# Optimization experiments

Hardware: AMD Instinct MI355X
Metric: run time of the kernel (lower is better)

Reference implementation:

```python
import jax, jax.numpy as jnp
import numpy as np

PAIR = 128
HID = 64
EPS = 1e-5


def _ln(x, w, b):
    mu = jnp.mean(x, axis=-1, keepdims=True)
    var = jnp.mean((x - mu) ** 2, axis=-1, keepdims=True)
    return (x - mu) * jax.lax.rsqrt(var + EPS) * w + b


def setup_inputs() -> dict:
    key = jax.random.key(0)
    ks = jax.random.split(key, 8)
    B, N = 1, 448
    s_in = 1.0 / np.sqrt(PAIR)
    s_h = 1.0 / np.sqrt(HID)
    return {
        "z": jax.random.normal(ks[0], (B, N, N, PAIR), jnp.float32),
        "z_mask": jnp.ones((B, N, N), jnp.float32),
        "ln_w": jnp.ones((PAIR,), jnp.float32),
        "ln_b": jnp.zeros((PAIR,), jnp.float32),
        "lnh_w": jnp.ones((HID,), jnp.float32),
        "lnh_b": jnp.zeros((HID,), jnp.float32),
        "g1_w": jax.random.uniform(ks[1], (PAIR, HID), jnp.float32, -s_in, s_in),
        "g1_b": jnp.zeros((HID,), jnp.float32),
        "g2_w": jax.random.uniform(ks[2], (PAIR, HID), jnp.float32, -s_in, s_in),
        "g2_b": jnp.zeros((HID,), jnp.float32),
        "l1_w": jax.random.uniform(ks[3], (PAIR, HID), jnp.float32, -s_in, s_in),
        "l1_b": jnp.zeros((HID,), jnp.float32),
        "l2_w": jax.random.uniform(ks[4], (PAIR, HID), jnp.float32, -s_in, s_in),
        "l2_b": jnp.zeros((HID,), jnp.float32),
        "eg_w": jax.random.uniform(ks[5], (PAIR, PAIR), jnp.float32, -s_in, s_in),
        "eg_b": jnp.zeros((PAIR,), jnp.float32),
        "out_w": jax.random.uniform(ks[6], (HID, PAIR), jnp.float32, -s_h, s_h),
        "out_b": jnp.zeros((PAIR,), jnp.float32),
    }


def reference(z, z_mask, ln_w, ln_b, lnh_w, lnh_b, g1_w, g1_b, g2_w, g2_b,
              l1_w, l1_b, l2_w, l2_b, eg_w, eg_b, out_w, out_b):
    m = z_mask[..., None]                      # [B,N,N,1]
    zn = _ln(z, ln_w, ln_b)                    # [B,N,N,P]
    ab1 = jax.nn.sigmoid(zn @ g1_w + g1_b) * (zn @ l1_w + l1_b) * m  # [B,N,N,H]
    ab2 = jax.nn.sigmoid(zn @ g2_w + g2_b) * (zn @ l2_w + l2_b) * m  # [B,N,N,H]
    # outgoing + incoming triangle products, per channel c
    block = (jnp.einsum('bikc,bjkc->bijc', ab1, ab2)
             + jnp.einsum('bkic,bkjc->bijc', ab1, ab2))              # [B,N,N,H]
    out = jax.nn.sigmoid(zn @ eg_w + eg_b) * (_ln(block, lnh_w, lnh_b) @ out_w + out_b) * m
    return out
```

## Files before the change

### kernel.cpp

```cpp
#include <hip/hip_runtime.h>
#include <stdint.h>

#define N 448
#define NN (N*N)
#define P 128
#define H 64
#define PN 512
#define CH (PN*N)

typedef __attribute__((ext_vector_type(8))) short bf16x8;
typedef __attribute__((ext_vector_type(4))) float f32x4;

__device__ __forceinline__ ushort f2bf(float f) {
    uint u = __builtin_bit_cast(uint, f);
    uint r = u + 0x7FFFu + ((u >> 16) & 1u);
    return (ushort)(r >> 16);
}
__device__ __forceinline__ float bf2f(ushort h) {
    uint u = ((uint)h) << 16;
    return __builtin_bit_cast(float, u);
}
__device__ __forceinline__ float sigmoidf(float x) {
    return 1.0f / (1.0f + __expf(-x));
}

__global__ void k_prep(const float* __restrict__ g1w, const float* __restrict__ l1w,
                       const float* __restrict__ g2w, const float* __restrict__ l2w,
                       const float* __restrict__ egw,
                       ushort* __restrict__ wfrag) {
    int idx = blockIdx.x*256 + threadIdx.x;
    for (int e = idx; e < 24*4*64*8; e += gridDim.x*256) {
        int b  = e & 7;
        int l  = (e >> 3) & 63;
        int ks = (e >> 9) & 3;
        int ct = e >> 11;
        int k   = ks*32 + 8*(l>>4) + b;
        int col = ct*16 + (l & 15);
        float v;
        if (col < 64)       v = g1w[k*64 + col];
        else if (col < 128) v = l1w[k*64 + col - 64];
        else if (col < 192) v = g2w[k*64 + col - 128];
        else if (col < 256) v = l2w[k*64 + col - 192];
        else                v = egw[k*128 + col - 256];
        wfrag[e] = f2bf(v);
    }
}

__global__ __launch_bounds__(256) void k_proj(
    const float* __restrict__ z, const float* __restrict__ mask,
    const float* __restrict__ lnw, const float* __restrict__ lnb,
    const float* __restrict__ g1b, const float* __restrict__ l1b,
    const float* __restrict__ g2b, const float* __restrict__ l2b,
    const float* __restrict__ egb,
    const ushort* __restrict__ wfrag,
    ushort* __restrict__ abt, ushort* __restrict__ gsig)
{
    __shared__ ushort zn[64*128];
    __shared__ ushort gs[64][136];
    const int t = threadIdx.x;
    const int w = t >> 6, l = t & 63;
    const int i = blockIdx.x / 7, j0 = (blockIdx.x % 7) * 64;

    {
        const int p = t >> 2;
        const int q = t & 3;
        const float* zp = z + (size_t)(i*N + j0 + p)*P + q*32;
        float4 v[8];
        #pragma unroll
        for (int x = 0; x < 8; ++x) v[x] = *(const float4*)(zp + x*4);
        float s = 0.f, sq = 0.f;
        #pragma unroll
        for (int x = 0; x < 8; ++x) {
            s  += v[x].x + v[x].y + v[x].z + v[x].w;
            sq += v[x].x*v[x].x + v[x].y*v[x].y + v[x].z*v[x].z + v[x].w*v[x].w;
        }
        s += __shfl_xor(s, 1);  sq += __shfl_xor(sq, 1);
        s += __shfl_xor(s, 2);  sq += __shfl_xor(sq, 2);
        float mu   = s * (1.0f/128.0f);
        float var  = sq * (1.0f/128.0f) - mu*mu;
        float rstd = rsqrtf(var + 1e-5f);
        #pragma unroll
        for (int cc = 0; cc < 4; ++cc) {
            int chunk = q*4 + cc;
            const float* lwp = lnw + chunk*8;
            const float* lbp = lnb + chunk*8;
            float4 lwa = *(const float4*)(lwp), lwb = *(const float4*)(lwp+4);
            float4 lba = *(const float4*)(lbp), lbb = *(const float4*)(lbp+4);
            float4 va = v[cc*2], vb = v[cc*2+1];
            float n0 = (va.x - mu)*rstd*lwa.x + lba.x;
            float n1 = (va.y - mu)*rstd*lwa.y + lba.y;
            float n2 = (va.z - mu)*rstd*lwa.z + lba.z;
            float n3 = (va.w - mu)*rstd*lwa.w + lba.w;
            float n4 = (vb.x - mu)*rstd*lwb.x + lbb.x;
            float n5 = (vb.y - mu)*rstd*lwb.y + lbb.y;
            float n6 = (vb.z - mu)*rstd*lwb.z + lbb.z;
            float n7 = (vb.w - mu)*rstd*lwb.w + lbb.w;
            uint4 pk;
            pk.x = (uint)f2bf(n0) | ((uint)f2bf(n1) << 16);
            pk.y = (uint)f2bf(n2) | ((uint)f2bf(n3) << 16);
            pk.z = (uint)f2bf(n4) | ((uint)f2bf(n5) << 16);
            pk.w = (uint)f2bf(n6) | ((uint)f2bf(n7) << 16);
            uint boff = (uint)p*256u + (((uint)(chunk ^ (p & 7)) & 15u) << 4);
            *(uint4*)((char*)zn + boff) = pk;
        }
    }
    __syncthreads();

    const int half = w & 1, pair = w >> 1;
    const uint lr = l & 15, lk = l >> 4;
    const int ct0 = pair*8 + half*2;
    int ctA[4] = { ct0, ct0 + 1, ct0 + 4, ct0 + 5 };

    const float* mrow = mask + (size_t)i*N + j0;

    f32x4 accA[4][4];
    #pragma unroll
    for (int a = 0; a < 4; ++a)
        #pragma unroll
        for (int b = 0; b < 4; ++b) accA[a][b] = (f32x4){0.f,0.f,0.f,0.f};

    #pragma unroll
    for (int ks = 0; ks < 4; ++ks) {
        bf16x8 af[4];
        #pragma unroll
        for (int mi = 0; mi < 4; ++mi) {
            uint row = mi*16u + lr;
            uint chunk = (uint)(ks*4) + lk;
            af[mi] = *(const bf16x8*)((const char*)zn + row*256u + (((chunk ^ (row & 7u)) & 15u) << 4));
        }
        #pragma unroll
        for (int c = 0; c < 4; ++c) {
            bf16x8 bfr = *(const bf16x8*)(wfrag + ((size_t)(ctA[c]*4 + ks)*64 + l)*8);
            #pragma unroll
            for (int mi = 0; mi < 4; ++mi)
                accA[mi][c] = __builtin_amdgcn_mfma_f32_16x16x32_bf16(af[mi], bfr, accA[mi][c], 0,0,0);
        }
    }

    {
        float biasA[4];
        #pragma unroll
        for (int c = 0; c < 4; ++c) {
            int col = ctA[c]*16 + (int)lr;
            float bv;
            if (col < 64)       bv = g1b[col];
            else if (col < 128) bv = l1b[col-64];
            else if (col < 192) bv = g2b[col-128];
            else                bv = l2b[col-192];
            biasA[c] = bv;
        }
        #pragma unroll
        for (int mi = 0; mi < 4; ++mi) {
            float mv[4];
            #pragma unroll
            for (int r = 0; r < 4; ++r) mv[r] = mrow[mi*16 + (int)lk*4 + r];
            #pragma unroll
            for (int pr = 0; pr < 2; ++pr) {
                int cc = (ctA[pr] - pair*8)*16 + (int)lr;
                ushort4 pk;
                float o0 = sigmoidf(accA[mi][pr][0] + biasA[pr]) * (accA[mi][pr+2][0] + biasA[pr+2]) * mv[0];
                float o1 = sigmoidf(accA[mi][pr][1] + biasA[pr]) * (accA[mi][pr+2][1] + biasA[pr+2]) * mv[1];
                float o2 = sigmoidf(accA[mi][pr][2] + biasA[pr]) * (accA[mi][pr+2][2] + biasA[pr+2]) * mv[2];
                float o3 = sigmoidf(accA[mi][pr][3] + biasA[pr]) * (accA[mi][pr+2][3] + biasA[pr+2]) * mv[3];
                pk.x = f2bf(o0); pk.y = f2bf(o1); pk.z = f2bf(o2); pk.w = f2bf(o3);
                size_t off = (size_t)(pair*64 + cc)*CH + (size_t)i*N + j0 + mi*16 + (int)lk*4;
                *(ushort4*)(abt + off) = pk;
            }
        }
    }

    f32x4 accB[4][2];
    #pragma unroll
    for (int a = 0; a < 4; ++a) { accB[a][0] = (f32x4){0,0,0,0}; accB[a][1] = (f32x4){0,0,0,0}; }

    #pragma unroll
    for (int ks = 0; ks < 4; ++ks) {
        bf16x8 af[4];
        #pragma unroll
        for (int mi = 0; mi < 4; ++mi) {
            uint row = mi*16u + lr;
            uint chunk = (uint)(ks*4) + lk;
            af[mi] = *(const bf16x8*)((const char*)zn + row*256u + (((chunk ^ (row & 7u)) & 15u) << 4));
        }
        #pragma unroll
        for (int e = 0; e < 2; ++e) {
            int ct = 16 + w*2 + e;
            bf16x8 bfr = *(const bf16x8*)(wfrag + ((size_t)(ct*4 + ks)*64 + l)*8);
            #pragma unroll
            for (int mi = 0; mi < 4; ++mi)
                accB[mi][e] = __builtin_amdgcn_mfma_f32_16x16x32_bf16(af[mi], bfr, accB[mi][e], 0,0,0);
        }
    }

    {
        float biasB[2];
        biasB[0] = egb[(16 + w*2)*16 + (int)lr - 256];
        biasB[1] = egb[(16 + w*2 + 1)*16 + (int)lr - 256];
        #pragma unroll
        for (int mi = 0; mi < 4; ++mi) {
            float mv[4];
            #pragma unroll
            for (int r = 0; r < 4; ++r) mv[r] = mrow[mi*16 + (int)lk*4 + r];
            #pragma unroll
            for (int e = 0; e < 2; ++e) {
                int cg = w*32 + e*16 + (int)lr;
                #pragma unroll
                for (int r = 0; r < 4; ++r) {
                    float sg = sigmoidf(accB[mi][e][r] + biasB[e]) * mv[r];
                    gs[mi*16 + (int)lk*4 + r][cg] = f2bf(sg);
                }
            }
        }
    }
    __syncthreads();

    {
        int p2 = t >> 2, q2 = t & 3;
        size_t pos = (size_t)(i*N + j0 + p2);
        #pragma unroll
        for (int s2 = 0; s2 < 4; ++s2) {
            uint4 vv = *(const uint4*)((const char*)&gs[p2][0] + q2*64 + s2*16);
            *(uint4*)(gsig + pos*128 + q2*32 + s2*8) = vv;
        }
    }
}

__global__ __launch_bounds__(256) void k_transpose(const ushort* __restrict__ abt,
                                                   ushort* __restrict__ abtt) {
    int bid = blockIdx.x;
    int tile = bid % 49, a = bid / 49;
    int y0 = (tile / 7) * 64, x0 = (tile % 7) * 64;
    const ushort* src = abt  + (size_t)a*CH;
    ushort*       dst = abtt + (size_t)a*CH;
    __shared__ ushort tl[64][68];
    int t = threadIdx.x;
    #pragma unroll
    for (int q = 0; q < 4; ++q) {
        int f = q*1024 + t*4;
        int r = f >> 6, c4 = f & 63;
        ushort4 v = *(const ushort4*)(src + (size_t)(y0 + r)*N + x0 + c4);
        tl[r][c4] = v.x; tl[r][c4+1] = v.y; tl[r][c4+2] = v.z; tl[r][c4+3] = v.w;
    }
    __syncthreads();
    #pragma unroll
    for (int q = 0; q < 4; ++q) {
        int f = q*1024 + t*4;
        int r = f >> 6, c4 = f & 63;
        ushort4 v;
        v.x = tl[c4][r]; v.y = tl[c4+1][r]; v.z = tl[c4+2][r]; v.w = tl[c4+3][r];
        *(ushort4*)(dst + (size_t)(x0 + r)*N + y0 + c4) = v;
    }
}

__global__ __launch_bounds__(256) void k_tri(const ushort* __restrict__ abt,
                                             const ushort* __restrict__ abtt,
                                             float* __restrict__ blk) {
    int bid = (blockIdx.x & 7)*128 + (blockIdx.x >> 3);
    const int c = bid >> 4;
    const int tij = bid & 15;
    const int i0 = (tij >> 2) * 128, j0 = (tij & 3) * 128;
    const int t = threadIdx.x, w = t >> 6, l = t & 63;
    const int wr = w >> 1, wc = w & 1;
    const uint lr = l & 15, lk = l >> 4;

    __shared__ ushort lds[4][128*64];

    const ushort* basep = (w >= 2) ? abtt : abt;
    const int chan = (w & 1) ? 64 + c : c;
    const int r0   = (w & 1) ? j0 : i0;
    const ushort* sbase = basep + (size_t)chan*CH + (size_t)r0*N;

    f32x4 acc[4][4];
    #pragma unroll
    for (int a = 0; a < 4; ++a)
        #pragma unroll
        for (int b = 0; b < 4; ++b) acc[a][b] = (f32x4){0.f,0.f,0.f,0.f};

    for (int kk = 0; kk < 7; ++kk) {
        __syncthreads();
        const ushort* sb = sbase + kk*64;
        #pragma unroll
        for (int q = 0; q < 16; ++q) {
            int r  = q*8 + (l >> 3);
            int ch = (l & 7) ^ (r & 7);
            const ushort* g = sb + (size_t)r*N + ch*8;
            __builtin_amdgcn_global_load_lds(
                (const __attribute__((address_space(1))) uint*)g,
                (__attribute__((address_space(3))) uint*)(&lds[w][q*512]),
                16, 0, 0);
        }
        __syncthreads();

        #pragma unroll
        for (int ks = 0; ks < 2; ++ks) {
            const uint chunk = (uint)(ks*4) + lk;
            bf16x8 a1[4], b1[4];
            #pragma unroll
            for (int x = 0; x < 4; ++x) {
                uint rowa = (uint)wr*64u + (uint)x*16u + lr;
                uint rowb = (uint)wc*64u + (uint)x*16u + lr;
                a1[x] = *(const bf16x8*)((const char*)lds[0] + rowa*128u + (((chunk ^ (rowa & 7u)) & 15u) << 4));
                b1[x] = *(const bf16x8*)((const char*)lds[1] + rowb*128u + (((chunk ^ (rowb & 7u)) & 15u) << 4));
            }
            #pragma unroll
            for (int mi = 0; mi < 4; ++mi)
                #pragma unroll
                for (int nj = 0; nj < 4; ++nj)
                    acc[mi][nj] = __builtin_amdgcn_mfma_f32_16x16x32_bf16(a1[mi], b1[nj], acc[mi][nj], 0,0,0);

            bf16x8 a2[4], b2[4];
            #pragma unroll
            for (int x = 0; x < 4; ++x) {
                uint rowa = (uint)wr*64u + (uint)x*16u + lr;
                uint rowb = (uint)wc*64u + (uint)x*16u + lr;
                a2[x] = *(const bf16x8*)((const char*)lds[2] + rowa*128u + (((chunk ^ (rowa & 7u)) & 15u) << 4));
                b2[x] = *(const bf16x8*)((const char*)lds[3] + rowb*128u + (((chunk ^ (rowb & 7u)) & 15u) << 4));
            }
            #pragma unroll
            for (int mi = 0; mi < 4; ++mi)
                #pragma unroll
                for (int nj = 0; nj < 4; ++nj)
                    acc[mi][nj] = __builtin_amdgcn_mfma_f32_16x16x32_bf16(a2[mi], b2[nj], acc[mi][nj], 0,0,0);
        }
    }

    #pragma unroll
    for (int mi = 0; mi < 4; ++mi) {
        int ib = i0 + wr*64 + mi*16 + (int)lk*4;
        #pragma unroll
        for (int nj = 0; nj < 4; ++nj) {
            int jb = j0 + wc*64 + nj*16 + (int)lr;
            if (jb < N) {
                #pragma unroll
                for (int r = 0; r < 4; ++r) {
                    int ii = ib + r;
                    if (ii < N) blk[(size_t)c*NN + (size_t)ii*N + jb] = acc[mi][nj][r];
                }
            }
        }
    }
}

__global__ __launch_bounds__(256) void k_out(const float* __restrict__ blk,
    const ushort* __restrict__ gsig,
    const float* __restrict__ lnhw, const float* __restrict__ lnhb,
    const float* __restrict__ outw, const float* __restrict__ outb,
    float* __restrict__ out)
{
    __shared__ float sblk[64][68];
    const int t = threadIdx.x;
    const int w = t >> 6, l = t & 63;
    const int pos0 = blockIdx.x * 64;

    #pragma unroll
    for (int q = 0; q < 4; ++q) {
        int flat = q*256 + t;
        int h = flat >> 4, f4 = flat & 15;
        float4 v = *(const float4*)(blk + (size_t)h*NN + pos0 + f4*4);
        sblk[f4*4+0][h] = v.x;
        sblk[f4*4+1][h] = v.y;
        sblk[f4*4+2][h] = v.z;
        sblk[f4*4+3][h] = v.w;
    }
    __syncthreads();

    {
        int p = w*16 + (l >> 2);
        int sub = l & 3;
        float vv[16];
        float s = 0.f, sq = 0.f;
        #pragma unroll
        for (int j = 0; j < 16; ++j) {
            float x = sblk[p][sub*16 + j];
            vv[j] = x; s += x; sq += x*x;
        }
        s += __shfl_xor(s, 1);  sq += __shfl_xor(sq, 1);
        s += __shfl_xor(s, 2);  sq += __shfl_xor(sq, 2);
        float mu   = s * (1.0f/64.0f);
        float var  = sq * (1.0f/64.0f) - mu*mu;
        float rstd = rsqrtf(var + 1e-5f);
        #pragma unroll
        for (int j = 0; j < 16; ++j) {
            float nv = (vv[j] - mu)*rstd*lnhw[sub*16+j] + lnhb[sub*16+j];
            sblk[p][sub*16 + j] = nv;
        }
    }
    __syncthreads();

    const int c4 = (t & 31) * 4;
    const int pg = t >> 5;
    float4 ob = *(const float4*)(outb + c4);

    #pragma unroll 1
    for (int hh = 0; hh < 2; ++hh) {
        const int prow = hh*32 + pg*4;
        float acc[4][4];
        #pragma unroll
        for (int j2 = 0; j2 < 4; ++j2)
            #pragma unroll
            for (int cc = 0; cc < 4; ++cc) acc[j2][cc] = 0.f;

        #pragma unroll 4
        for (int h4 = 0; h4 < 16; ++h4) {
            float4 wv[4];
            #pragma unroll
            for (int j = 0; j < 4; ++j)
                wv[j] = *(const float4*)(outw + (h4*4+j)*128 + c4);
            #pragma unroll
            for (int j2 = 0; j2 < 4; ++j2) {
                float4 av = *(const float4*)(&sblk[prow + j2][h4*4]);
                acc[j2][0] += av.x*wv[0].x + av.y*wv[1].x + av.z*wv[2].x + av.w*wv[3].x;
                acc[j2][1] += av.x*wv[0].y + av.y*wv[1].y + av.z*wv[2].y + av.w*wv[3].y;
                acc[j2][2] += av.x*wv[0].z + av.y*wv[1].z + av.z*wv[2].z + av.w*wv[3].z;
                acc[j2][3] += av.x*wv[0].w + av.y*wv[1].w + av.z*wv[2].w + av.w*wv[3].w;
            }
        }

        #pragma unroll
        for (int j2 = 0; j2 < 4; ++j2) {
            size_t pos = (size_t)(pos0 + prow + j2);
            ushort4 gv = *(const ushort4*)(gsig + pos*128 + c4);
            float4 res;
            res.x = bf2f(gv.x) * (acc[j2][0] + ob.x);
            res.y = bf2f(gv.y) * (acc[j2][1] + ob.y);
            res.z = bf2f(gv.z) * (acc[j2][2] + ob.z);
            res.w = bf2f(gv.w) * (acc[j2][3] + ob.w);
            *(float4*)(out + pos*128 + c4) = res;
        }
    }
}

extern "C" void kernel_launch(void* const* d_in, const int* in_sizes, int n_in,
                              void* d_out, int out_size, void* d_ws, size_t ws_size,
                              hipStream_t stream) {
    const float* z    = (const float*)d_in[0];
    const float* mask = (const float*)d_in[1];
    const float* lnw  = (const float*)d_in[2];
    const float* lnb  = (const float*)d_in[3];
    const float* lnhw = (const float*)d_in[4];
    const float* lnhb = (const float*)d_in[5];
    const float* g1w  = (const float*)d_in[6];
    const float* g1b  = (const float*)d_in[7];
    const float* g2w  = (const float*)d_in[8];
    const float* g2b  = (const float*)d_in[9];
    const float* l1w  = (const float*)d_in[10];
    const float* l1b  = (const float*)d_in[11];
    const float* l2w  = (const float*)d_in[12];
    const float* l2b  = (const float*)d_in[13];
    const float* egw  = (const float*)d_in[14];
    const float* egb  = (const float*)d_in[15];
    const float* outw = (const float*)d_in[16];
    const float* outb = (const float*)d_in[17];

    char* ws = (char*)d_ws;
    const size_t SZ_AB = (size_t)2*64*CH*2;
    const size_t SZ_G  = (size_t)NN*128*2;
    const size_t SZ_BL = (size_t)64*NN*4;
    ushort* abt    = (ushort*)ws;
    ushort* abtt   = (ushort*)(ws + SZ_AB);
    ushort* gsig   = (ushort*)(ws + 2*SZ_AB);
    float*  blkb   = (float*) (ws + 2*SZ_AB + SZ_G);
    ushort* wfrag  = (ushort*)(ws + 2*SZ_AB + SZ_G + SZ_BL);

    k_prep<<<32, 256, 0, stream>>>(g1w, l1w, g2w, l2w, egw, wfrag);
    k_proj<<<3136, 256, 0, stream>>>(z, mask, lnw, lnb, g1b, l1b, g2b, l2b, egb, wfrag, abt, gsig);
    k_transpose<<<128*49, 256, 0, stream>>>(abt, abtt);
    k_tri<<<64*16, 256, 0, stream>>>(abt, abtt, blkb);
    k_out<<<NN/64, 256, 0, stream>>>(blkb, gsig, lnhw, lnhb, outw, outb, (float*)d_out);
}
```

Before: 289.9 us.

## Split projection accumulators into sub-passes and double k_tri waves per block

In k_proj, the gate/linear projection is rewritten as two sequential sub-passes, each holding 8 accumulators instead of 16. A-fragments are loaded per MFMA rather than kept in arrays, and the eg projection is restructured the same way, which lowers register pressure. In k_tri the block grows from 256 to 512 threads: each wave computes a 64x32 output tile, and pairs of waves split the LDS staging of each operand. The aim is higher occupancy and more latency hiding, at the cost of reloading zn fragments more often and using smaller per-wave tiles with less register reuse.

```diff
diff --git a/kernel.cpp b/kernel.cpp
--- a/kernel.cpp
+++ b/kernel.cpp
@@ -108,94 +108,73 @@
 
     const int half = w & 1, pair = w >> 1;
     const uint lr = l & 15, lk = l >> 4;
-    const int ct0 = pair*8 + half*2;
-    int ctA[4] = { ct0, ct0 + 1, ct0 + 4, ct0 + 5 };
-
     const float* mrow = mask + (size_t)i*N + j0;
-
-    f32x4 accA[4][4];
-    #pragma unroll
-    for (int a = 0; a < 4; ++a)
-        #pragma unroll
-        for (int b = 0; b < 4; ++b) accA[a][b] = (f32x4){0.f,0.f,0.f,0.f};
-
-    #pragma unroll
-    for (int ks = 0; ks < 4; ++ks) {
-        bf16x8 af[4];
-        #pragma unroll
-        for (int mi = 0; mi < 4; ++mi) {
-            uint row = mi*16u + lr;
-            uint chunk = (uint)(ks*4) + lk;
-            af[mi] = *(const bf16x8*)((const char*)zn + row*256u + (((chunk ^ (row & 7u)) & 15u) << 4));
-        }
-        #pragma unroll
-        for (int c = 0; c < 4; ++c) {
-            bf16x8 bfr = *(const bf16x8*)(wfrag + ((size_t)(ctA[c]*4 + ks)*64 + l)*8);
-            #pragma unroll
-            for (int mi = 0; mi < 4; ++mi)
-                accA[mi][c] = __builtin_amdgcn_mfma_f32_16x16x32_bf16(af[mi], bfr, accA[mi][c], 0,0,0);
-        }
-    }
-
-    {
-        float biasA[4];
-        #pragma unroll
-        for (int c = 0; c < 4; ++c) {
-            int col = ctA[c]*16 + (int)lr;
-            float bv;
-            if (col < 64)       bv = g1b[col];
-            else if (col < 128) bv = l1b[col-64];
-            else if (col < 192) bv = g2b[col-128];
-            else                bv = l2b[col-192];
-            biasA[c] = bv;
-        }
+    const float* gb = pair ? g2b : g1b;
+    const float* lb = pair ? l2b : l1b;
+
+    #pragma unroll 1
+    for (int sub = 0; sub < 2; ++sub) {
+        const int ctg = pair*8 + half*2 + sub;
+        const int ctl = ctg + 4;
+        f32x4 ag[4], al[4];
+        #pragma unroll
+        for (int mi = 0; mi < 4; ++mi) { ag[mi] = (f32x4){0,0,0,0}; al[mi] = (f32x4){0,0,0,0}; }
+
+        #pragma unroll
+        for (int ks = 0; ks < 4; ++ks) {
+            bf16x8 bg = *(const bf16x8*)(wfrag + ((size_t)(ctg*4 + ks)*64 + l)*8);
+            bf16x8 blf = *(const bf16x8*)(wfrag + ((size_t)(ctl*4 + ks)*64 + l)*8);
+            #pragma unroll
+            for (int mi = 0; mi < 4; ++mi) {
+                uint row = mi*16u + lr;
+                uint chunk = (uint)(ks*4) + lk;
+                bf16x8 af = *(const bf16x8*)((const char*)zn + row*256u + (((chunk ^ (row & 7u)) & 15u) << 4));
+                ag[mi] = __builtin_amdgcn_mfma_f32_16x16x32_bf16(af, bg,  ag[mi], 0,0,0);
+                al[mi] = __builtin_amdgcn_mfma_f32_16x16x32_bf16(af, blf, al[mi], 0,0,0);
+            }
+        }
+
+        const int cidx = (half*2 + sub)*16 + (int)lr;
+        const float gbias = gb[cidx];
+        const float lbias = lb[cidx];
         #pragma unroll
         for (int mi = 0; mi < 4; ++mi) {
             float mv[4];
             #pragma unroll
             for (int r = 0; r < 4; ++r) mv[r] = mrow[mi*16 + (int)lk*4 + r];
-            #pragma unroll
-            for (int pr = 0; pr < 2; ++pr) {
-                int cc = (ctA[pr] - pair*8)*16 + (int)lr;
-                ushort4 pk;
-                float o0 = sigmoidf(accA[mi][pr][0] + biasA[pr]) * (accA[mi][pr+2][0] + biasA[pr+2]) * mv[0];
-                float o1 = sigmoidf(accA[mi][pr][1] + biasA[pr]) * (accA[mi][pr+2][1] + biasA[pr+2]) * mv[1];
-                float o2 = sigmoidf(accA[mi][pr][2] + biasA[pr]) * (accA[mi][pr+2][2] + biasA[pr+2]) * mv[2];
-                float o3 = sigmoidf(accA[mi][pr][3] + biasA[pr]) * (accA[mi][pr+2][3] + biasA[pr+2]) * mv[3];
-                pk.x = f2bf(o0); pk.y = f2bf(o1); pk.z = f2bf(o2); pk.w = f2bf(o3);
-                size_t off = (size_t)(pair*64 + cc)*CH + (size_t)i*N + j0 + mi*16 + (int)lk*4;
-                *(ushort4*)(abt + off) = pk;
-            }
-        }
-    }
-
-    f32x4 accB[4][2];
-    #pragma unroll
-    for (int a = 0; a < 4; ++a) { accB[a][0] = (f32x4){0,0,0,0}; accB[a][1] = (f32x4){0,0,0,0}; }
-
-    #pragma unroll
-    for (int ks = 0; ks < 4; ++ks) {
-        bf16x8 af[4];
-        #pragma unroll
-        for (int mi = 0; mi < 4; ++mi) {
-            uint row = mi*16u + lr;
-            uint chunk = (uint)(ks*4) + lk;
-            af[mi] = *(const bf16x8*)((const char*)zn + row*256u + (((chunk ^ (row & 7u)) & 15u) << 4));
-        }
-        #pragma unroll
-        for (int e = 0; e < 2; ++e) {
-            int ct = 16 + w*2 + e;
-            bf16x8 bfr = *(const bf16x8*)(wfrag + ((size_t)(ct*4 + ks)*64 + l)*8);
-            #pragma unroll
-            for (int mi = 0; mi < 4; ++mi)
-                accB[mi][e] = __builtin_amdgcn_mfma_f32_16x16x32_bf16(af[mi], bfr, accB[mi][e], 0,0,0);
+            ushort4 pk;
+            float o0 = sigmoidf(ag[mi][0] + gbias) * (al[mi][0] + lbias) * mv[0];
+            float o1 = sigmoidf(ag[mi][1] + gbias) * (al[mi][1] + lbias) * mv[1];
+            float o2 = sigmoidf(ag[mi][2] + gbias) * (al[mi][2] + lbias) * mv[2];
+            float o3 = sigmoidf(ag[mi][3] + gbias) * (al[mi][3] + lbias) * mv[3];
+            pk.x = f2bf(o0); pk.y = f2bf(o1); pk.z = f2bf(o2); pk.w = f2bf(o3);
+            size_t off = (size_t)(pair*64 + cidx)*CH + (size_t)i*N + j0 + mi*16 + (int)lk*4;
+            *(ushort4*)(abt + off) = pk;
         }
     }
 
     {
+        f32x4 ae[4][2];
+        #pragma unroll
+        for (int mi = 0; mi < 4; ++mi) { ae[mi][0] = (f32x4){0,0,0,0}; ae[mi][1] = (f32x4){0,0,0,0}; }
+
+        #pragma unroll
+        for (int ks = 0; ks < 4; ++ks) {
+            bf16x8 b0 = *(const bf16x8*)(wfrag + ((size_t)((16 + w*2)*4 + ks)*64 + l)*8);
+            bf16x8 b1 = *(const bf16x8*)(wfrag + ((size_t)((17 + w*2)*4 + ks)*64 + l)*8);
+            #pragma unroll
+            for (int mi = 0; mi < 4; ++mi) {
+                uint row = mi*16u + lr;
+                uint chunk = (uint)(ks*4) + lk;
+                bf16x8 af = *(const bf16x8*)((const char*)zn + row*256u + (((chunk ^ (row & 7u)) & 15u) << 4));
+                ae[mi][0] = __builtin_amdgcn_mfma_f32_16x16x32_bf16(af, b0, ae[mi][0], 0,0,0);
+                ae[mi][1] = __builtin_amdgcn_mfma_f32_16x16x32_bf16(af, b1, ae[mi][1], 0,0,0);
+            }
+        }
+
         float biasB[2];
-        biasB[0] = egb[(16 + w*2)*16 + (int)lr - 256];
-        biasB[1] = egb[(16 + w*2 + 1)*16 + (int)lr - 256];
+        biasB[0] = egb[w*32 + (int)lr];
+        biasB[1] = egb[w*32 + 16 + (int)lr];
         #pragma unroll
         for (int mi = 0; mi < 4; ++mi) {
             float mv[4];
@@ -206,7 +185,7 @@
                 int cg = w*32 + e*16 + (int)lr;
                 #pragma unroll
                 for (int r = 0; r < 4; ++r) {
-                    float sg = sigmoidf(accB[mi][e][r] + biasB[e]) * mv[r];
+                    float sg = sigmoidf(ae[mi][e][r] + biasB[e]) * mv[r];
                     gs[mi*16 + (int)lk*4 + r][cg] = f2bf(sg);
                 }
             }
@@ -252,7 +231,7 @@
     }
 }
 
-__global__ __launch_bounds__(256) void k_tri(const ushort* __restrict__ abt,
+__global__ __launch_bounds__(512) void k_tri(const ushort* __restrict__ abt,
                                              const ushort* __restrict__ abtt,
                                              float* __restrict__ blk) {
     int bid = (blockIdx.x & 7)*128 + (blockIdx.x >> 3);
@@ -260,33 +239,33 @@
     const int tij = bid & 15;
     const int i0 = (tij >> 2) * 128, j0 = (tij & 3) * 128;
     const int t = threadIdx.x, w = t >> 6, l = t & 63;
-    const int wr = w >> 1, wc = w & 1;
+    const int wr = w >> 2, wc = w & 3;
     const uint lr = l & 15, lk = l >> 4;
 
     __shared__ ushort lds[4][128*64];
 
-    const ushort* basep = (w >= 2) ? abtt : abt;
-    const int chan = (w & 1) ? 64 + c : c;
-    const int r0   = (w & 1) ? j0 : i0;
+    const int tt = w >> 1;
+    const ushort* basep = (tt >= 2) ? abtt : abt;
+    const int chan = (tt & 1) ? 64 + c : c;
+    const int r0   = (tt & 1) ? j0 : i0;
     const ushort* sbase = basep + (size_t)chan*CH + (size_t)r0*N;
-
-    f32x4 acc[4][4];
+    const int rhalf = (w & 1) * 64;
+
+    f32x4 acc[4][2];
     #pragma unroll
-    for (int a = 0; a < 4; ++a)
-        #pragma unroll
-        for (int b = 0; b < 4; ++b) acc[a][b] = (f32x4){0.f,0.f,0.f,0.f};
+    for (int a = 0; a < 4; ++a) { acc[a][0] = (f32x4){0,0,0,0}; acc[a][1] = (f32x4){0,0,0,0}; }
 
     for (int kk = 0; kk < 7; ++kk) {
         __syncthreads();
         const ushort* sb = sbase + kk*64;
         #pragma unroll
-        for (int q = 0; q < 16; ++q) {
-            int r  = q*8 + (l >> 3);
+        for (int q = 0; q < 8; ++q) {
+            int r  = rhalf + q*8 + (l >> 3);
             int ch = (l & 7) ^ (r & 7);
             const ushort* g = sb + (size_t)r*N + ch*8;
             __builtin_amdgcn_global_load_lds(
                 (const __attribute__((address_space(1))) uint*)g,
-                (__attribute__((address_space(3))) uint*)(&lds[w][q*512]),
+                (__attribute__((address_space(3))) uint*)(&lds[tt][rhalf*64 + q*512]),
                 16, 0, 0);
         }
         __syncthreads();
@@ -294,32 +273,38 @@
         #pragma unroll
         for (int ks = 0; ks < 2; ++ks) {
             const uint chunk = (uint)(ks*4) + lk;
-            bf16x8 a1[4], b1[4];
+            bf16x8 a1[4], b1[2];
             #pragma unroll
             for (int x = 0; x < 4; ++x) {
                 uint rowa = (uint)wr*64u + (uint)x*16u + lr;
-                uint rowb = (uint)wc*64u + (uint)x*16u + lr;
                 a1[x] = *(const bf16x8*)((const char*)lds[0] + rowa*128u + (((chunk ^ (rowa & 7u)) & 15u) << 4));
+            }
+            #pragma unroll
+            for (int x = 0; x < 2; ++x) {
+                uint rowb = (uint)wc*32u + (uint)x*16u + lr;
                 b1[x] = *(const bf16x8*)((const char*)lds[1] + rowb*128u + (((chunk ^ (rowb & 7u)) & 15u) << 4));
             }
             #pragma unroll
             for (int mi = 0; mi < 4; ++mi)
                 #pragma unroll
-                for (int nj = 0; nj < 4; ++nj)
+                for (int nj = 0; nj < 2; ++nj)
                     acc[mi][nj] = __builtin_amdgcn_mfma_f32_16x16x32_bf16(a1[mi], b1[nj], acc[mi][nj], 0,0,0);
 
-            bf16x8 a2[4], b2[4];
+            bf16x8 a2[4], b2[2];
             #pragma unroll
             for (int x = 0; x < 4; ++x) {
                 uint rowa = (uint)wr*64u + (uint)x*16u + lr;
-                uint rowb = (uint)wc*64u + (uint)x*16u + lr;
                 a2[x] = *(const bf16x8*)((const char*)lds[2] + rowa*128u + (((chunk ^ (rowa & 7u)) & 15u) << 4));
+            }
+            #pragma unroll
+            for (int x = 0; x < 2; ++x) {
+                uint rowb = (uint)wc*32u + (uint)x*16u + lr;
                 b2[x] = *(const bf16x8*)((const char*)lds[3] + rowb*128u + (((chunk ^ (rowb & 7u)) & 15u) << 4));
             }
             #pragma unroll
             for (int mi = 0; mi < 4; ++mi)
                 #pragma unroll
-                for (int nj = 0; nj < 4; ++nj)
+                for (int nj = 0; nj < 2; ++nj)
                     acc[mi][nj] = __builtin_amdgcn_mfma_f32_16x16x32_bf16(a2[mi], b2[nj], acc[mi][nj], 0,0,0);
         }
     }
@@ -328,8 +313,8 @@
     for (int mi = 0; mi < 4; ++mi) {
         int ib = i0 + wr*64 + mi*16 + (int)lk*4;
         #pragma unroll
-        for (int nj = 0; nj < 4; ++nj) {
-            int jb = j0 + wc*64 + nj*16 + (int)lr;
+        for (int nj = 0; nj < 2; ++nj) {
+            int jb = j0 + wc*32 + nj*16 + (int)lr;
             if (jb < N) {
                 #pragma unroll
                 for (int r = 0; r < 4; ++r) {
@@ -465,6 +450,6 @@
     k_prep<<<32, 256, 0, stream>>>(g1w, l1w, g2w, l2w, egw, wfrag);
     k_proj<<<3136, 256, 0, stream>>>(z, mask, lnw, lnb, g1b, l1b, g2b, l2b, egb, wfrag, abt, gsig);
     k_transpose<<<128*49, 256, 0, stream>>>(abt, abtt);
-    k_tri<<<64*16, 256, 0, stream>>>(abt, abtt, blkb);
+    k_tri<<<64*16, 512, 0, stream>>>(abt, abtt, blkb);
     k_out<<<NN/64, 256, 0, stream>>>(blkb, gsig, lnhw, lnhb, outw, outb, (float*)d_out);
 }
```

New measurement: 297.7 us. +2.7%, slower.
